# Kernel optimization log

Hardware: AMD Instinct MI355X
Metric: run time of the kernel (lower is better)

## Reference

```python
import jax, jax.numpy as jnp
import numpy as np

N, NFEAT, NHID, NCLASS, NHEADS = 4096, 512, 64, 128, 8
ALPHA = 0.2
NEG = -9e15


def leaky(x):
    return jnp.where(x > 0, x, ALPHA * x)


def setup_inputs() -> dict:
    key = jax.random.key(0)
    k = jax.random.split(key, 6)
    x = jax.random.normal(k[0], (N, NFEAT), dtype=jnp.float32)
    adj = jax.random.randint(k[1], (N, N), 0, 2, dtype=jnp.int32)
    # per-head params (xavier-ish scale)
    W = jax.random.normal(k[2], (NHEADS, NFEAT, NHID), dtype=jnp.float32) * (1.414 * (2.0 / (NFEAT + NHID)) ** 0.5)
    a = jax.random.normal(k[3], (NHEADS, 2 * NHID), dtype=jnp.float32) * (1.414 * (2.0 / (2 * NHID + 1)) ** 0.5)
    W_out = jax.random.normal(k[4], (NHEADS * NHID, NCLASS), dtype=jnp.float32) * (1.414 * (2.0 / (NHEADS * NHID + NCLASS)) ** 0.5)
    a_out = jax.random.normal(k[5], (2 * NCLASS,), dtype=jnp.float32) * (1.414 * (2.0 / (2 * NCLASS + 1)) ** 0.5)
    return {"x": x, "adj": adj, "W": W, "a": a, "W_out": W_out, "a_out": a_out}


def _gat_layer_multihead(x, adj_mask, W, a):
    # x: [N,F_in], W: [H,F_in,F_out], a: [H,2*F_out]
    h = jnp.einsum('nf,hfo->hno', x, W)           # [H,N,F_out]
    Fo = W.shape[-1]
    a1, a2 = a[:, :Fo], a[:, Fo:]                  # [H,F_out] each
    fi = jnp.einsum('hno,ho->hn', h, a1)           # score contribution of node i
    fj = jnp.einsum('hno,ho->hn', h, a2)
    e = leaky(fi[:, :, None] + fj[:, None, :])     # [H,N,N] == leakyrelu(a . [h_i||h_j])
    e = jnp.where(adj_mask[None], e, NEG)
    att = jax.nn.softmax(e, axis=-1)
    return jnp.einsum('hij,hjo->hio', att, h)      # [H,N,F_out]


def reference(x, adj, W, a, W_out, a_out):
    adj_mask = adj > 0
    # multi-head hidden layer, concat heads (dropout is identity in eval mode)
    hp = _gat_layer_multihead(x, adj_mask, W, a)            # [H,N,NHID]
    xcat = jnp.transpose(hp, (1, 0, 2)).reshape(N, NHEADS * NHID)
    # output attention layer (single head)
    out = _gat_layer_multihead(xcat, adj_mask, W_out[None], a_out[None])[0]  # [N,NCLASS]
    out = jax.nn.elu(out)
    return jax.nn.log_softmax(out, axis=1)
```

## Files before the change

### kernel.cpp

```cpp
#include <hip/hip_runtime.h>
#include <hip/hip_bf16.h>

#define NNODE 4096

typedef __attribute__((ext_vector_type(8))) short bf16x8;
typedef __attribute__((ext_vector_type(4))) float f32x4;
typedef __attribute__((ext_vector_type(4))) unsigned short us4;
typedef __attribute__((ext_vector_type(8))) unsigned short us8;

__device__ __forceinline__ unsigned short f2bf(float x) {
  __hip_bfloat16 b = __float2bfloat16(x);
  return __builtin_bit_cast(unsigned short, b);
}

__global__ __launch_bounds__(256) void packadj(
    const int* __restrict__ adj, unsigned long long* __restrict__ mask) {
  size_t wid = (size_t)blockIdx.x * 4 + (threadIdx.x >> 6);
  int v = adj[wid * 64 + (threadIdx.x & 63)];
  unsigned long long b = __ballot(v != 0);
  if ((threadIdx.x & 63) == 0) mask[wid] = b;
}

__global__ __launch_bounds__(256) void transpose_bf16(
    const float* __restrict__ src, short* __restrict__ dst, int Nr, int Fsrc) {
  __shared__ float tile[64][68];
  const int t  = threadIdx.x;
  const int n0 = blockIdx.x * 64, o0 = blockIdx.y * 64;
  const int h  = blockIdx.z;
  const float* S = src + ((size_t)h * Nr + n0) * Fsrc + o0;
  short* D = dst + ((size_t)h * Fsrc + o0) * Nr + n0;
  const int r = t >> 2, cs = (t & 3) * 16;
  #pragma unroll
  for (int k2 = 0; k2 < 4; ++k2) {
    float4 v = *(const float4*)&S[(size_t)r * Fsrc + cs + k2 * 4];
    *(float4*)&tile[r][cs + k2 * 4] = v;
  }
  __syncthreads();
  const int o = t >> 2, ns = (t & 3) * 16;
  us8 u0, u1;
  #pragma unroll
  for (int e = 0; e < 8; ++e) u0[e] = f2bf(tile[ns + e][o]);
  #pragma unroll
  for (int e = 0; e < 8; ++e) u1[e] = f2bf(tile[ns + 8 + e][o]);
  *(us8*)&D[(size_t)o * Nr + ns]     = u0;
  *(us8*)&D[(size_t)o * Nr + ns + 8] = u1;
}

__global__ __launch_bounds__(256) void gemm_mfma(
    const float* __restrict__ A, const short* __restrict__ Wt,
    short* __restrict__ hTout, int M, int K, int Nfull) {
  __shared__ short As[64][72];
  const int t  = threadIdx.x;
  const int lane = t & 63;
  const int w  = t >> 6;
  const int i0 = blockIdx.x * 64;
  const int c0 = blockIdx.y * 64;
  const int h  = blockIdx.z;
  const short* Bh = Wt + ((size_t)h * Nfull + c0) * K;
  short*       Hh = hTout + (size_t)h * Nfull * M;

  const int R0 = (w >> 1) * 32;
  const int C0 = (w & 1) * 32;
  const int lr = lane & 15;
  const int lk = lane >> 4;

  const int arow = t >> 2;
  const int aseg = (t & 3) * 16;

  f32x4 acc[2][2] = {};

  const short* b00p = &Bh[(size_t)(C0 + lr) * K + lk * 8];
  const short* b10p = &Bh[(size_t)(C0 + 16 + lr) * K + lk * 8];

  bf16x8 bc[4];
  bc[0] = *(const bf16x8*)(b00p);
  bc[1] = *(const bf16x8*)(b10p);
  bc[2] = *(const bf16x8*)(b00p + 32);
  bc[3] = *(const bf16x8*)(b10p + 32);

  for (int k0 = 0; k0 < K; k0 += 64) {
    {
      const float* src = &A[(size_t)(i0 + arow) * K + k0 + aseg];
      float4 v0 = *(const float4*)(src);
      float4 v1 = *(const float4*)(src + 4);
      float4 v2 = *(const float4*)(src + 8);
      float4 v3 = *(const float4*)(src + 12);
      us8 u0, u1;
      u0[0] = f2bf(v0.x); u0[1] = f2bf(v0.y); u0[2] = f2bf(v0.z); u0[3] = f2bf(v0.w);
      u0[4] = f2bf(v1.x); u0[5] = f2bf(v1.y); u0[6] = f2bf(v1.z); u0[7] = f2bf(v1.w);
      u1[0] = f2bf(v2.x); u1[1] = f2bf(v2.y); u1[2] = f2bf(v2.z); u1[3] = f2bf(v2.w);
      u1[4] = f2bf(v3.x); u1[5] = f2bf(v3.y); u1[6] = f2bf(v3.z); u1[7] = f2bf(v3.w);
      *(us8*)&As[arow][aseg]     = u0;
      *(us8*)&As[arow][aseg + 8] = u1;
    }
    bf16x8 bn[4];
    {
      int kn = (k0 + 64 < K) ? (k0 + 64) : k0;
      bn[0] = *(const bf16x8*)(b00p + kn);
      bn[1] = *(const bf16x8*)(b10p + kn);
      bn[2] = *(const bf16x8*)(b00p + kn + 32);
      bn[3] = *(const bf16x8*)(b10p + kn + 32);
    }
    __syncthreads();
    #pragma unroll
    for (int kc = 0; kc < 64; kc += 32) {
      bf16x8 a0 = *(const bf16x8*)&As[R0 + lr][kc + lk * 8];
      bf16x8 a1 = *(const bf16x8*)&As[R0 + 16 + lr][kc + lk * 8];
      bf16x8 b0 = bc[(kc >> 5) * 2 + 0];
      bf16x8 b1 = bc[(kc >> 5) * 2 + 1];
      acc[0][0] = __builtin_amdgcn_mfma_f32_16x16x32_bf16(a0, b0, acc[0][0], 0, 0, 0);
      acc[0][1] = __builtin_amdgcn_mfma_f32_16x16x32_bf16(a0, b1, acc[0][1], 0, 0, 0);
      acc[1][0] = __builtin_amdgcn_mfma_f32_16x16x32_bf16(a1, b0, acc[1][0], 0, 0, 0);
      acc[1][1] = __builtin_amdgcn_mfma_f32_16x16x32_bf16(a1, b1, acc[1][1], 0, 0, 0);
    }
    bc[0] = bn[0]; bc[1] = bn[1]; bc[2] = bn[2]; bc[3] = bn[3];
    __syncthreads();
  }

  #pragma unroll
  for (int fa = 0; fa < 2; ++fa) {
    #pragma unroll
    for (int fb = 0; fb < 2; ++fb) {
      int col  = c0 + C0 + fb * 16 + lr;
      int rowb = i0 + R0 + fa * 16 + lk * 4;
      us4 pk;
      #pragma unroll
      for (int reg = 0; reg < 4; ++reg) pk[reg] = f2bf(acc[fa][fb][reg]);
      *(us4*)&Hh[(size_t)col * M + rowb] = pk;
    }
  }
}

template<int F>
__global__ __launch_bounds__(256) void wa_kernel(
    const float* __restrict__ W, const float* __restrict__ a,
    float* __restrict__ wa) {
  const int gid  = blockIdx.x * 4 + (threadIdx.x >> 6);
  const int lane = threadIdx.x & 63;
  const int h = gid >> 9;
  const int k = gid & 511;
  const float* wrow = W + ((size_t)h * 512 + k) * F;
  const float* ah = a + h * 2 * F;
  float v1 = 0.f, v2 = 0.f;
  #pragma unroll
  for (int o = lane; o < F; o += 64) {
    float wv = wrow[o];
    v1 += wv * ah[o];
    v2 += wv * ah[F + o];
  }
  #pragma unroll
  for (int off = 32; off; off >>= 1) {
    v1 += __shfl_xor(v1, off);
    v2 += __shfl_xor(v2, off);
  }
  if (lane == 0) {
    wa[((size_t)h * 2 + 0) * 512 + k] = v1;
    wa[((size_t)h * 2 + 1) * 512 + k] = v2;
  }
}

__global__ __launch_bounds__(256) void fidot8(
    const float* __restrict__ X, const float* __restrict__ wa,
    float* __restrict__ fi, float* __restrict__ fj,
    float* __restrict__ eiP, float* __restrict__ eiN,
    float* __restrict__ ejP, float* __restrict__ ejN) {
  __shared__ float sw[8192];
  for (int idx = threadIdx.x; idx < 8192; idx += 256) sw[idx] = wa[idx];
  __syncthreads();
  const int n    = blockIdx.x * 4 + (threadIdx.x >> 6);
  const int lane = threadIdx.x & 63;
  const float* xr = X + (size_t)n * 512;
  float v[16] = {};
  #pragma unroll
  for (int it = 0; it < 8; ++it) {
    int k = lane + it * 64;
    float xv = xr[k];
    #pragma unroll
    for (int hh = 0; hh < 8; ++hh) {
      v[2 * hh]     += xv * sw[(2 * hh) * 512 + k];
      v[2 * hh + 1] += xv * sw[(2 * hh + 1) * 512 + k];
    }
  }
  #pragma unroll
  for (int off = 32; off; off >>= 1)
    #pragma unroll
    for (int i = 0; i < 16; ++i) v[i] += __shfl_xor(v[i], off);
  if (lane == 0) {
    #pragma unroll
    for (int hh = 0; hh < 8; ++hh) {
      int idx = hh * NNODE + n;
      float f1 = v[2 * hh], f2 = v[2 * hh + 1];
      fi[idx] = f1;  fj[idx] = f2;
      eiP[idx] = __expf(f1); eiN[idx] = __expf(0.2f * f1);
      ejP[idx] = __expf(f2); ejN[idx] = __expf(0.2f * f2);
    }
  }
}

template<int OT, int JLEN>
__global__ __launch_bounds__(256) void pv_split(
    const short* __restrict__ hT, const float* __restrict__ fi,
    const float* __restrict__ eiP, const float* __restrict__ eiN,
    const float* __restrict__ fj, const float* __restrict__ ejP,
    const float* __restrict__ ejN, const unsigned long long* __restrict__ mask,
    float* __restrict__ pnum, float* __restrict__ pl, int Fh) {
  __shared__ short hTl[OT][64][72];
  __shared__ float fjL[64], ejPL[64], ejNL[64];

  const int t      = threadIdx.x;
  const int lane   = t & 63;
  const int w      = t >> 6;
  const int i0     = blockIdx.x * 64;
  const int chunk  = blockIdx.y;
  const int nchunk = gridDim.y;
  const int h      = blockIdx.z;
  const int hN     = h * NNODE;
  const short* hTs = hT + (size_t)h * Fh * NNODE;

  const int lr = lane & 15;
  const int lk = lane >> 4;
  const int arow = i0 + w * 16 + lr;
  const float thr  = -fi[hN + arow];
  const float eiPr = eiP[hN + arow];
  const float eiNr = eiN[hN + arow];
  const unsigned long long* mrow = mask + (size_t)arow * (NNODE / 64);

  f32x4 acc[OT][4] = {};
  float lsum = 0.0f;

  const int jbase = chunk * JLEN;
  for (int jt = 0; jt < JLEN; jt += 64) {
    const int j0 = jbase + jt;
    {
      const int o = t >> 2, seg = t & 3;
      #pragma unroll
      for (int ot = 0; ot < OT; ++ot) {
        const short* src = hTs + (size_t)(ot * 64 + o) * NNODE + j0 + seg * 16;
        float4 v0 = *(const float4*)(src);
        float4 v1 = *(const float4*)(src + 8);
        *(float4*)&hTl[ot][o][seg * 16]     = v0;
        *(float4*)&hTl[ot][o][seg * 16 + 8] = v1;
      }
    }
    if (t < 64) {
      fjL[t]  = fj[hN + j0 + t];
      ejPL[t] = ejP[hN + j0 + t];
      ejNL[t] = ejN[hN + j0 + t];
    }
    __syncthreads();

    const unsigned long long mw = mrow[j0 >> 6];
    #pragma unroll
    for (int kk = 0; kk < 2; ++kk) {
      const int kc = kk * 32;
      const int kb = kc + lk * 8;
      float4 fj0 = *(const float4*)&fjL[kb];
      float4 fj1 = *(const float4*)&fjL[kb + 4];
      float4 eP0 = *(const float4*)&ejPL[kb];
      float4 eP1 = *(const float4*)&ejPL[kb + 4];
      float4 eN0 = *(const float4*)&ejNL[kb];
      float4 eN1 = *(const float4*)&ejNL[kb + 4];
      const unsigned int mb = (unsigned int)(mw >> kb) & 0xFFu;
      float pv[8];
      pv[0] = (fj0.x > thr) ? eiPr * eP0.x : eiNr * eN0.x;
      pv[1] = (fj0.y > thr) ? eiPr * eP0.y : eiNr * eN0.y;
      pv[2] = (fj0.z > thr) ? eiPr * eP0.z : eiNr * eN0.z;
      pv[3] = (fj0.w > thr) ? eiPr * eP0.w : eiNr * eN0.w;
      pv[4] = (fj1.x > thr) ? eiPr * eP1.x : eiNr * eN1.x;
      pv[5] = (fj1.y > thr) ? eiPr * eP1.y : eiNr * eN1.y;
      pv[6] = (fj1.z > thr) ? eiPr * eP1.z : eiNr * eN1.z;
      pv[7] = (fj1.w > thr) ? eiPr * eP1.w : eiNr * eN1.w;
      us8 af;
      #pragma unroll
      for (int e = 0; e < 8; ++e) {
        float p = (mb & (1u << e)) ? pv[e] : 0.0f;
        lsum += p;
        af[e] = f2bf(p);
      }
      bf16x8 a = __builtin_bit_cast(bf16x8, af);
      #pragma unroll
      for (int ot = 0; ot < OT; ++ot) {
        #pragma unroll
        for (int c = 0; c < 4; ++c) {
          bf16x8 b = *(const bf16x8*)&hTl[ot][c * 16 + lr][kb];
          acc[ot][c] = __builtin_amdgcn_mfma_f32_16x16x32_bf16(a, b, acc[ot][c], 0, 0, 0);
        }
      }
    }
    __syncthreads();
  }

  lsum += __shfl_xor(lsum, 16);
  lsum += __shfl_xor(lsum, 32);
  if (lk == 0)
    pl[(size_t)(h * nchunk + chunk) * NNODE + arow] = lsum;

  float* pout = pnum + ((size_t)(h * nchunk + chunk) * NNODE + i0) * (OT * 64);
  #pragma unroll
  for (int ot = 0; ot < OT; ++ot) {
    #pragma unroll
    for (int c = 0; c < 4; ++c) {
      #pragma unroll
      for (int reg = 0; reg < 4; ++reg) {
        int row = w * 16 + lk * 4 + reg;
        int col = ot * 64 + c * 16 + lr;
        pout[(size_t)row * (OT * 64) + col] = acc[ot][c][reg];
      }
    }
  }
}

__global__ __launch_bounds__(256) void combine1_fidot(
    const float* __restrict__ pnum, const float* __restrict__ pl,
    const float* __restrict__ wa2, float* __restrict__ xcat,
    float* __restrict__ fi2, float* __restrict__ fj2,
    float* __restrict__ eiP2, float* __restrict__ eiN2,
    float* __restrict__ ejP2, float* __restrict__ ejN2) {
  const int n = blockIdx.x, t = threadIdx.x;
  float d1 = 0.f, d2 = 0.f;
  #pragma unroll
  for (int rep = 0; rep < 2; ++rep) {
    int col = t + rep * 256;
    int h = col >> 6, o = col & 63;
    float s = 0.f, L = 0.f;
    #pragma unroll
    for (int c = 0; c < 2; ++c) {
      s += pnum[((size_t)(h * 2 + c) * NNODE + n) * 64 + o];
      L += pl[(size_t)(h * 2 + c) * NNODE + n];
    }
    float xv = s / L;
    xcat[(size_t)n * 512 + col] = xv;
    d1 += xv * wa2[col];
    d2 += xv * wa2[512 + col];
  }
  #pragma unroll
  for (int off = 32; off; off >>= 1) {
    d1 += __shfl_xor(d1, off);
    d2 += __shfl_xor(d2, off);
  }
  __shared__ float red[2][4];
  if ((t & 63) == 0) { red[0][t >> 6] = d1; red[1][t >> 6] = d2; }
  __syncthreads();
  if (t == 0) {
    float f1 = red[0][0] + red[0][1] + red[0][2] + red[0][3];
    float f2 = red[1][0] + red[1][1] + red[1][2] + red[1][3];
    fi2[n] = f1;  fj2[n] = f2;
    eiP2[n] = __expf(f1); eiN2[n] = __expf(0.2f * f1);
    ejP2[n] = __expf(f2); ejN2[n] = __expf(0.2f * f2);
  }
}

__global__ __launch_bounds__(128) void combine2_final(
    const float* __restrict__ pnum, const float* __restrict__ pl,
    float* __restrict__ dout) {
  const int n = blockIdx.x, t = threadIdx.x;
  float s = 0.f, L = 0.f;
  #pragma unroll
  for (int c = 0; c < 8; ++c) {
    s += pnum[((size_t)c * NNODE + n) * 128 + t];
    L += pl[(size_t)c * NNODE + n];
  }
  float v = s / L;
  float e = v > 0.f ? v : (__expf(v) - 1.0f);
  float mx = e;
  #pragma unroll
  for (int off = 32; off; off >>= 1) mx = fmaxf(mx, __shfl_xor(mx, off));
  __shared__ float r2[2];
  if ((t & 63) == 0) r2[t >> 6] = mx;
  __syncthreads();
  mx = fmaxf(r2[0], r2[1]);
  float sm = __expf(e - mx);
  #pragma unroll
  for (int off = 32; off; off >>= 1) sm += __shfl_xor(sm, off);
  __shared__ float s2[2];
  if ((t & 63) == 0) s2[t >> 6] = sm;
  __syncthreads();
  float sum = s2[0] + s2[1];
  dout[(size_t)n * 128 + t] = e - mx - __logf(sum);
}

extern "C" void kernel_launch(void* const* d_in, const int* in_sizes, int n_in,
                              void* d_out, int out_size, void* d_ws, size_t ws_size,
                              hipStream_t stream) {
  const float* x     = (const float*)d_in[0];
  const int*   adj   = (const int*)d_in[1];
  const float* W     = (const float*)d_in[2];
  const float* a     = (const float*)d_in[3];
  const float* W_out = (const float*)d_in[4];
  const float* a_out = (const float*)d_in[5];
  float* out = (float*)d_out;

  float* ws = (float*)d_ws;
  unsigned long long* mask = (unsigned long long*)ws;
  float* xcat = ws + 524288;
  short* hT   = (short*)(xcat + 2097152);
  float* pnum = (float*)(((short*)hT) + 2097152);
  float* pl   = pnum + 4194304;
  short* Wt1  = (short*)(pl + 131072);
  short* Wt2  = Wt1 + 262144;
  float* wa1  = (float*)(Wt2 + 65536);
  float* wa2  = wa1 + 8192;
  float* fi1  = wa2 + 1024;
  float* fj1  = fi1 + 32768;
  float* eiP1 = fj1 + 32768;
  float* eiN1 = eiP1 + 32768;
  float* ejP1 = eiN1 + 32768;
  float* ejN1 = ejP1 + 32768;
  float* fi2  = ejN1 + 32768;
  float* fj2  = fi2 + 4096;
  float* eiP2 = fj2 + 4096;
  float* eiN2 = eiP2 + 4096;
  float* ejP2 = eiN2 + 4096;
  float* ejN2 = ejP2 + 4096;

  packadj<<<dim3(NNODE * NNODE / 64 / 4), 256, 0, stream>>>(adj, mask);
  transpose_bf16<<<dim3(8, 1, 8), 256, 0, stream>>>(W, Wt1, 512, 64);
  transpose_bf16<<<dim3(8, 2, 1), 256, 0, stream>>>(W_out, Wt2, 512, 128);
  wa_kernel<64><<<dim3(8 * 512 / 4), 256, 0, stream>>>(W, a, wa1);
  wa_kernel<128><<<dim3(512 / 4), 256, 0, stream>>>(W_out, a_out, wa2);

  gemm_mfma<<<dim3(64, 1, 8), 256, 0, stream>>>(x, Wt1, hT, 4096, 512, 64);
  fidot8<<<dim3(4096 / 4), 256, 0, stream>>>(x, wa1, fi1, fj1, eiP1, eiN1, ejP1, ejN1);
  pv_split<1, 2048><<<dim3(64, 2, 8), 256, 0, stream>>>(hT, fi1, eiP1, eiN1, fj1, ejP1, ejN1, mask, pnum, pl, 64);
  combine1_fidot<<<dim3(NNODE), 256, 0, stream>>>(pnum, pl, wa2, xcat, fi2, fj2, eiP2, eiN2, ejP2, ejN2);

  gemm_mfma<<<dim3(64, 2, 1), 256, 0, stream>>>(xcat, Wt2, hT, 4096, 512, 128);
  pv_split<2, 512><<<dim3(64, 8, 1), 256, 0, stream>>>(hT, fi2, eiP2, eiN2, fj2, ejP2, ejN2, mask, pnum, pl, 128);
  combine2_final<<<dim3(NNODE), 128, 0, stream>>>(pnum, pl, out);
}
```

Baseline: 248.0 us.

## Pre-convert GEMM inputs to bf16, use max-based leaky exp, MFMA row sums

```diff
diff --git a/kernel.cpp b/kernel.cpp
--- a/kernel.cpp
+++ b/kernel.cpp
@@ -47,7 +47,7 @@
 }
 
 __global__ __launch_bounds__(256) void gemm_mfma(
-    const float* __restrict__ A, const short* __restrict__ Wt,
+    const short* __restrict__ A, const short* __restrict__ Wt,
     short* __restrict__ hTout, int M, int K, int Nfull) {
   __shared__ short As[64][72];
   const int t  = threadIdx.x;
@@ -80,16 +80,9 @@
 
   for (int k0 = 0; k0 < K; k0 += 64) {
     {
-      const float* src = &A[(size_t)(i0 + arow) * K + k0 + aseg];
-      float4 v0 = *(const float4*)(src);
-      float4 v1 = *(const float4*)(src + 4);
-      float4 v2 = *(const float4*)(src + 8);
-      float4 v3 = *(const float4*)(src + 12);
-      us8 u0, u1;
-      u0[0] = f2bf(v0.x); u0[1] = f2bf(v0.y); u0[2] = f2bf(v0.z); u0[3] = f2bf(v0.w);
-      u0[4] = f2bf(v1.x); u0[5] = f2bf(v1.y); u0[6] = f2bf(v1.z); u0[7] = f2bf(v1.w);
-      u1[0] = f2bf(v2.x); u1[1] = f2bf(v2.y); u1[2] = f2bf(v2.z); u1[3] = f2bf(v2.w);
-      u1[4] = f2bf(v3.x); u1[5] = f2bf(v3.y); u1[6] = f2bf(v3.z); u1[7] = f2bf(v3.w);
+      const short* src = &A[(size_t)(i0 + arow) * K + k0 + aseg];
+      us8 u0 = *(const us8*)(src);
+      us8 u1 = *(const us8*)(src + 8);
       *(us8*)&As[arow][aseg]     = u0;
       *(us8*)&As[arow][aseg + 8] = u1;
     }
@@ -161,7 +154,7 @@
 
 __global__ __launch_bounds__(256) void fidot8(
     const float* __restrict__ X, const float* __restrict__ wa,
-    float* __restrict__ fi, float* __restrict__ fj,
+    short* __restrict__ xbf,
     float* __restrict__ eiP, float* __restrict__ eiN,
     float* __restrict__ ejP, float* __restrict__ ejN) {
   __shared__ float sw[8192];
@@ -175,6 +168,7 @@
   for (int it = 0; it < 8; ++it) {
     int k = lane + it * 64;
     float xv = xr[k];
+    xbf[(size_t)n * 512 + k] = f2bf(xv);
     #pragma unroll
     for (int hh = 0; hh < 8; ++hh) {
       v[2 * hh]     += xv * sw[(2 * hh) * 512 + k];
@@ -190,7 +184,6 @@
     for (int hh = 0; hh < 8; ++hh) {
       int idx = hh * NNODE + n;
       float f1 = v[2 * hh], f2 = v[2 * hh + 1];
-      fi[idx] = f1;  fj[idx] = f2;
       eiP[idx] = __expf(f1); eiN[idx] = __expf(0.2f * f1);
       ejP[idx] = __expf(f2); ejN[idx] = __expf(0.2f * f2);
     }
@@ -199,13 +192,13 @@
 
 template<int OT, int JLEN>
 __global__ __launch_bounds__(256) void pv_split(
-    const short* __restrict__ hT, const float* __restrict__ fi,
+    const short* __restrict__ hT,
     const float* __restrict__ eiP, const float* __restrict__ eiN,
-    const float* __restrict__ fj, const float* __restrict__ ejP,
-    const float* __restrict__ ejN, const unsigned long long* __restrict__ mask,
+    const float* __restrict__ ejP, const float* __restrict__ ejN,
+    const unsigned long long* __restrict__ mask,
     float* __restrict__ pnum, float* __restrict__ pl, int Fh) {
   __shared__ short hTl[OT][64][72];
-  __shared__ float fjL[64], ejPL[64], ejNL[64];
+  __shared__ float ejPL[64], ejNL[64];
 
   const int t      = threadIdx.x;
   const int lane   = t & 63;
@@ -220,13 +213,17 @@
   const int lr = lane & 15;
   const int lk = lane >> 4;
   const int arow = i0 + w * 16 + lr;
-  const float thr  = -fi[hN + arow];
   const float eiPr = eiP[hN + arow];
   const float eiNr = eiN[hN + arow];
   const unsigned long long* mrow = mask + (size_t)arow * (NNODE / 64);
 
+  us8 onesu;
+  #pragma unroll
+  for (int e = 0; e < 8; ++e) onesu[e] = 0x3F80;
+  const bf16x8 ones = __builtin_bit_cast(bf16x8, onesu);
+
   f32x4 acc[OT][4] = {};
-  float lsum = 0.0f;
+  f32x4 accL = {};
 
   const int jbase = chunk * JLEN;
   for (int jt = 0; jt < JLEN; jt += 64) {
@@ -243,7 +240,6 @@
       }
     }
     if (t < 64) {
-      fjL[t]  = fj[hN + j0 + t];
       ejPL[t] = ejP[hN + j0 + t];
       ejNL[t] = ejN[hN + j0 + t];
     }
@@ -252,32 +248,27 @@
     const unsigned long long mw = mrow[j0 >> 6];
     #pragma unroll
     for (int kk = 0; kk < 2; ++kk) {
-      const int kc = kk * 32;
-      const int kb = kc + lk * 8;
-      float4 fj0 = *(const float4*)&fjL[kb];
-      float4 fj1 = *(const float4*)&fjL[kb + 4];
+      const int kb = kk * 32 + lk * 8;
       float4 eP0 = *(const float4*)&ejPL[kb];
       float4 eP1 = *(const float4*)&ejPL[kb + 4];
       float4 eN0 = *(const float4*)&ejNL[kb];
       float4 eN1 = *(const float4*)&ejNL[kb + 4];
       const unsigned int mb = (unsigned int)(mw >> kb) & 0xFFu;
       float pv[8];
-      pv[0] = (fj0.x > thr) ? eiPr * eP0.x : eiNr * eN0.x;
-      pv[1] = (fj0.y > thr) ? eiPr * eP0.y : eiNr * eN0.y;
-      pv[2] = (fj0.z > thr) ? eiPr * eP0.z : eiNr * eN0.z;
-      pv[3] = (fj0.w > thr) ? eiPr * eP0.w : eiNr * eN0.w;
-      pv[4] = (fj1.x > thr) ? eiPr * eP1.x : eiNr * eN1.x;
-      pv[5] = (fj1.y > thr) ? eiPr * eP1.y : eiNr * eN1.y;
-      pv[6] = (fj1.z > thr) ? eiPr * eP1.z : eiNr * eN1.z;
-      pv[7] = (fj1.w > thr) ? eiPr * eP1.w : eiNr * eN1.w;
+      pv[0] = fmaxf(eiPr * eP0.x, eiNr * eN0.x);
+      pv[1] = fmaxf(eiPr * eP0.y, eiNr * eN0.y);
+      pv[2] = fmaxf(eiPr * eP0.z, eiNr * eN0.z);
+      pv[3] = fmaxf(eiPr * eP0.w, eiNr * eN0.w);
+      pv[4] = fmaxf(eiPr * eP1.x, eiNr * eN1.x);
+      pv[5] = fmaxf(eiPr * eP1.y, eiNr * eN1.y);
+      pv[6] = fmaxf(eiPr * eP1.z, eiNr * eN1.z);
+      pv[7] = fmaxf(eiPr * eP1.w, eiNr * eN1.w);
       us8 af;
       #pragma unroll
-      for (int e = 0; e < 8; ++e) {
-        float p = (mb & (1u << e)) ? pv[e] : 0.0f;
-        lsum += p;
-        af[e] = f2bf(p);
-      }
+      for (int e = 0; e < 8; ++e)
+        af[e] = f2bf((mb & (1u << e)) ? pv[e] : 0.0f);
       bf16x8 a = __builtin_bit_cast(bf16x8, af);
+      accL = __builtin_amdgcn_mfma_f32_16x16x32_bf16(a, ones, accL, 0, 0, 0);
       #pragma unroll
       for (int ot = 0; ot < OT; ++ot) {
         #pragma unroll
@@ -290,10 +281,11 @@
     __syncthreads();
   }
 
-  lsum += __shfl_xor(lsum, 16);
-  lsum += __shfl_xor(lsum, 32);
-  if (lk == 0)
-    pl[(size_t)(h * nchunk + chunk) * NNODE + arow] = lsum;
+  if (lr == 0) {
+    #pragma unroll
+    for (int reg = 0; reg < 4; ++reg)
+      pl[(size_t)(h * nchunk + chunk) * NNODE + i0 + w * 16 + lk * 4 + reg] = accL[reg];
+  }
 
   float* pout = pnum + ((size_t)(h * nchunk + chunk) * NNODE + i0) * (OT * 64);
   #pragma unroll
@@ -312,8 +304,7 @@
 
 __global__ __launch_bounds__(256) void combine1_fidot(
     const float* __restrict__ pnum, const float* __restrict__ pl,
-    const float* __restrict__ wa2, float* __restrict__ xcat,
-    float* __restrict__ fi2, float* __restrict__ fj2,
+    const float* __restrict__ wa2, short* __restrict__ xcatbf,
     float* __restrict__ eiP2, float* __restrict__ eiN2,
     float* __restrict__ ejP2, float* __restrict__ ejN2) {
   const int n = blockIdx.x, t = threadIdx.x;
@@ -329,7 +320,7 @@
       L += pl[(size_t)(h * 2 + c) * NNODE + n];
     }
     float xv = s / L;
-    xcat[(size_t)n * 512 + col] = xv;
+    xcatbf[(size_t)n * 512 + col] = f2bf(xv);
     d1 += xv * wa2[col];
     d2 += xv * wa2[512 + col];
   }
@@ -344,7 +335,6 @@
   if (t == 0) {
     float f1 = red[0][0] + red[0][1] + red[0][2] + red[0][3];
     float f2 = red[1][0] + red[1][1] + red[1][2] + red[1][3];
-    fi2[n] = f1;  fj2[n] = f2;
     eiP2[n] = __expf(f1); eiN2[n] = __expf(0.2f * f1);
     ejP2[n] = __expf(f2); ejN2[n] = __expf(0.2f * f2);
   }
@@ -392,23 +382,20 @@
 
   float* ws = (float*)d_ws;
   unsigned long long* mask = (unsigned long long*)ws;
-  float* xcat = ws + 524288;
-  short* hT   = (short*)(xcat + 2097152);
-  float* pnum = (float*)(((short*)hT) + 2097152);
+  short* xbf    = (short*)(ws + 524288);
+  short* xcatbf = xbf + 2097152;
+  short* hT     = xcatbf + 2097152;
+  float* pnum = (float*)(hT + 2097152);
   float* pl   = pnum + 4194304;
   short* Wt1  = (short*)(pl + 131072);
   short* Wt2  = Wt1 + 262144;
   float* wa1  = (float*)(Wt2 + 65536);
   float* wa2  = wa1 + 8192;
-  float* fi1  = wa2 + 1024;
-  float* fj1  = fi1 + 32768;
-  float* eiP1 = fj1 + 32768;
+  float* eiP1 = wa2 + 1024;
   float* eiN1 = eiP1 + 32768;
   float* ejP1 = eiN1 + 32768;
   float* ejN1 = ejP1 + 32768;
-  float* fi2  = ejN1 + 32768;
-  float* fj2  = fi2 + 4096;
-  float* eiP2 = fj2 + 4096;
+  float* eiP2 = ejN1 + 32768;
   float* eiN2 = eiP2 + 4096;
   float* ejP2 = eiN2 + 4096;
   float* ejN2 = ejP2 + 4096;
@@ -419,12 +406,12 @@
   wa_kernel<64><<<dim3(8 * 512 / 4), 256, 0, stream>>>(W, a, wa1);
   wa_kernel<128><<<dim3(512 / 4), 256, 0, stream>>>(W_out, a_out, wa2);
 
-  gemm_mfma<<<dim3(64, 1, 8), 256, 0, stream>>>(x, Wt1, hT, 4096, 512, 64);
-  fidot8<<<dim3(4096 / 4), 256, 0, stream>>>(x, wa1, fi1, fj1, eiP1, eiN1, ejP1, ejN1);
-  pv_split<1, 2048><<<dim3(64, 2, 8), 256, 0, stream>>>(hT, fi1, eiP1, eiN1, fj1, ejP1, ejN1, mask, pnum, pl, 64);
-  combine1_fidot<<<dim3(NNODE), 256, 0, stream>>>(pnum, pl, wa2, xcat, fi2, fj2, eiP2, eiN2, ejP2, ejN2);
-
-  gemm_mfma<<<dim3(64, 2, 1), 256, 0, stream>>>(xcat, Wt2, hT, 4096, 512, 128);
-  pv_split<2, 512><<<dim3(64, 8, 1), 256, 0, stream>>>(hT, fi2, eiP2, eiN2, fj2, ejP2, ejN2, mask, pnum, pl, 128);
+  fidot8<<<dim3(4096 / 4), 256, 0, stream>>>(x, wa1, xbf, eiP1, eiN1, ejP1, ejN1);
+  gemm_mfma<<<dim3(64, 1, 8), 256, 0, stream>>>(xbf, Wt1, hT, 4096, 512, 64);
+  pv_split<1, 2048><<<dim3(64, 2, 8), 256, 0, stream>>>(hT, eiP1, eiN1, ejP1, ejN1, mask, pnum, pl, 64);
+  combine1_fidot<<<dim3(NNODE), 256, 0, stream>>>(pnum, pl, wa2, xcatbf, eiP2, eiN2, ejP2, ejN2);
+
+  gemm_mfma<<<dim3(64, 2, 1), 256, 0, stream>>>(xcatbf, Wt2, hT, 4096, 512, 128);
+  pv_split<2, 512><<<dim3(64, 8, 1), 256, 0, stream>>>(hT, eiP2, eiN2, ejP2, ejN2, mask, pnum, pl, 128);
   combine2_final<<<dim3(NNODE), 128, 0, stream>>>(pnum, pl, out);
 }
```

Result: no change. 244.1 us (-1.6%).
